# Kernel tuning notes

Hardware: AMD Instinct MI355X
Metric: run time of the kernel (lower is better)

The kernel has to match this reference:

```python
import jax, jax.numpy as jnp
import numpy as np

N = 100000   # nodes
E = 1600000  # edges (self-loop free by construction)
B = 512      # graphs in batch
F = 128      # input node features
HID = 128    # hidden dim
HEADS = 4
CH = HID // HEADS  # 32
EPS_BN = 1e-5


def setup_inputs() -> dict:
    key = jax.random.key(0)
    ks = jax.random.split(key, 24)
    x = jax.random.normal(ks[0], (N, F), jnp.float32)
    dst = jax.random.randint(ks[1], (E,), 0, N)
    off = jax.random.randint(ks[2], (E,), 1, N)
    src = (dst + off) % N  # guaranteed no self loops
    edge_index = jnp.stack([src, dst]).astype(jnp.int32)
    batch = jnp.sort(jax.random.randint(ks[3], (N,), 0, B)).astype(jnp.int32)
    g = lambda k, shape, fan: jax.random.normal(k, shape, jnp.float32) / np.sqrt(fan)
    return {
        "x": x, "edge_index": edge_index, "batch": batch,
        "W_in": g(ks[4], (F, HID), F), "b_in": jnp.zeros((HID,), jnp.float32),
        "lin_w": g(ks[5], (2, HID, HID), HID),
        "att_src": g(ks[6], (2, HEADS, CH), CH),
        "att_dst": g(ks[7], (2, HEADS, CH), CH),
        "conv_b": jnp.zeros((2, HID), jnp.float32),
        "lin_w_last": g(ks[8], (HID, HID), HID),
        "att_src_last": g(ks[9], (HID,), HID),
        "att_dst_last": g(ks[10], (HID,), HID),
        "b_last": jnp.zeros((HID,), jnp.float32),
        "bn_g": jnp.ones((3, HID), jnp.float32) + 0.1 * jax.random.normal(ks[11], (3, HID), jnp.float32),
        "bn_b": 0.1 * jax.random.normal(ks[12], (3, HID), jnp.float32),
        "bn_m": 0.1 * jax.random.normal(ks[13], (3, HID), jnp.float32),
        "bn_v": 0.5 + jax.random.uniform(ks[14], (3, HID), jnp.float32),
        "ro_w1": g(ks[15], (HID, HID // 2), HID),
        "ro_b1": jnp.zeros((HID // 2,), jnp.float32),
        "ro_w2": g(ks[16], (HID // 2, 1), HID // 2),
        "ro_b2": jnp.zeros((1,), jnp.float32),
    }


def _gat_conv(h, src, dst, W, a_src, a_dst, bias, concat):
    """PyG GATConv (shared lin for src/dst, add_self_loops=True, eval mode)."""
    n = h.shape[0]
    heads, ch = a_src.shape
    xs = (h @ W).reshape(n, heads, ch)              # [N,H,C]
    al_s = jnp.sum(xs * a_src, axis=-1)             # [N,H]
    al_d = jnp.sum(xs * a_dst, axis=-1)             # [N,H]
    loop = jnp.arange(n, dtype=src.dtype)
    src_f = jnp.concatenate([src, loop])
    dst_f = jnp.concatenate([dst, loop])
    e = jax.nn.leaky_relu(al_s[src_f] + al_d[dst_f], 0.2)   # [E+N,H]
    m = jax.ops.segment_max(e, dst_f, num_segments=n)       # dest-grouped softmax
    ee = jnp.exp(e - m[dst_f])
    z = jax.ops.segment_sum(ee, dst_f, num_segments=n)
    alpha = ee / (z[dst_f] + 1e-16)                          # [E+N,H]
    out = jax.ops.segment_sum(alpha[:, :, None] * xs[src_f], dst_f, num_segments=n)
    out = out.reshape(n, heads * ch) if concat else jnp.mean(out, axis=1)
    return out + bias


def _bn_eval(h, g, b, m, v):
    return (h - m) * (g / jnp.sqrt(v + EPS_BN)) + b


def _seg_softmax(scores, seg, num_segments):
    m = jax.ops.segment_max(scores, seg, num_segments=num_segments)
    e = jnp.exp(scores - m[seg])
    z = jax.ops.segment_sum(e, seg, num_segments=num_segments)
    return e / z[seg]


def reference(x, edge_index, batch, W_in, b_in, lin_w, att_src, att_dst, conv_b,
              lin_w_last, att_src_last, att_dst_last, b_last,
              bn_g, bn_b, bn_m, bn_v, ro_w1, ro_b1, ro_w2, ro_b2):
    src, dst = edge_index[0], edge_index[1]
    h = x @ W_in + b_in                                       # input_proj
    # first num_layers-1 multi-head concat layers
    for i in range(2):
        h_new = _gat_conv(h, src, dst, lin_w[i], att_src[i], att_dst[i], conv_b[i], True)
        h_new = jax.nn.elu(_bn_eval(h_new, bn_g[i], bn_b[i], bn_m[i], bn_v[i]))
        h = h + h_new                                         # residual (shapes match)
    # final single-head layer, concat=False
    h_new = _gat_conv(h, src, dst, lin_w_last, att_src_last[None, :], att_dst_last[None, :], b_last, False)
    h_new = jax.nn.elu(_bn_eval(h_new, bn_g[2], bn_b[2], bn_m[2], bn_v[2]))
    h = h + h_new
    # attention readout + per-graph softmax over atoms
    atom_scores = (jnp.tanh(h @ ro_w1 + ro_b1) @ ro_w2 + ro_b2)[:, 0]   # [N]
    atom_attention = _seg_softmax(atom_scores, batch, B)
    # attention-weighted add pool
    graph_emb = jax.ops.segment_sum(h * atom_attention[:, None], batch, num_segments=B)
    return graph_emb, atom_attention
```

## Files before the change

kernel.cpp:

```cpp
#include <hip/hip_runtime.h>
#include <math.h>
#include <stdint.h>

#define BSZ 512
#define BSH 9
#define NBKT_MAX 256

typedef __attribute__((ext_vector_type(8))) short bf16x8;
typedef __attribute__((ext_vector_type(4))) float f32x4;

static __device__ __forceinline__ uint32_t f2bf(float x) {
    uint32_t u = __float_as_uint(x);
    return (u + 0x7fffu + ((u >> 16) & 1u)) >> 16;
}
static __device__ __forceinline__ float bflo(uint32_t v) { return __uint_as_float(v << 16); }
static __device__ __forceinline__ float bfhi(uint32_t v) { return __uint_as_float(v & 0xffff0000u); }
static __device__ __forceinline__ void split2(float x, short& hi, short& lo) {
    uint32_t hb = f2bf(x);
    float hf = __uint_as_float(hb << 16);
    uint32_t lb = f2bf(x - hf);
    hi = (short)hb; lo = (short)lb;
}

__global__ __launch_bounds__(256) void k_bucket(const int* __restrict__ src, const int* __restrict__ dst,
                                                int* __restrict__ bcur, uint32_t* __restrict__ bucketed,
                                                int e, int cap) {
    __shared__ int hist[NBKT_MAX];
    __shared__ int cur[NBKT_MAX];
    int t = threadIdx.x;
    hist[t] = 0;
    __syncthreads();
    int base = blockIdx.x * 8192;
#pragma unroll 4
    for (int i = 0; i < 32; ++i) {
        int ei = base + i * 256 + t;
        if (ei < e) atomicAdd(&hist[dst[ei] >> BSH], 1);
    }
    __syncthreads();
    int hc = hist[t];
    cur[t] = (hc > 0) ? atomicAdd(&bcur[t], hc) : 0;
    __syncthreads();
#pragma unroll 4
    for (int i = 0; i < 32; ++i) {
        int ei = base + i * 256 + t;
        if (ei < e) {
            int d = dst[ei], s = src[ei];
            int b = d >> BSH;
            int p = atomicAdd(&cur[b], 1);
            if (p < (b + 1) * cap)
                bucketed[p] = ((uint32_t)(d & (BSZ - 1)) << 23) | (uint32_t)s;
        }
    }
}
__global__ __launch_bounds__(256) void k_bcount(const int* __restrict__ bcur, const uint32_t* __restrict__ bucketed,
                                                int* __restrict__ cnt, int n, int cap) {
    __shared__ int lf[BSZ];
    int b = blockIdx.x, t = threadIdx.x;
    int n0 = b << BSH;
    int nn = min(BSZ, n - n0);
    for (int i = t; i < nn; i += 256) lf[i] = 0;
    __syncthreads();
    int cb = min(bcur[b] - b * cap, cap);
    const uint32_t* ba = bucketed + (size_t)b * cap;
    for (int i = t; i < cb; i += 256) atomicAdd(&lf[ba[i] >> 23], 1);
    __syncthreads();
    for (int i = t; i < nn; i += 256) cnt[n0 + i] = lf[i] + 1;
}
__global__ __launch_bounds__(256) void k_scan1(const int* __restrict__ cnt, int* __restrict__ bsum, int n) {
    __shared__ int sd[256];
    int base = blockIdx.x * 1024, t = threadIdx.x;
    int s = 0;
#pragma unroll
    for (int i = 0; i < 4; ++i) {
        int idx = base + t * 4 + i;
        if (idx < n) s += (cnt[idx] + 3) & ~3;
    }
    sd[t] = s; __syncthreads();
    for (int o = 128; o; o >>= 1) {
        if (t < o) sd[t] += sd[t + o];
        __syncthreads();
    }
    if (t == 0) bsum[blockIdx.x] = sd[0];
}
__global__ void k_scan2(int* __restrict__ bsum, int nb) {
    __shared__ int sd[128];
    int t = threadIdx.x;
    int v = (t < nb) ? bsum[t] : 0;
    sd[t] = v; __syncthreads();
    for (int o = 1; o < 128; o <<= 1) {
        int u = (t >= o) ? sd[t - o] : 0;
        __syncthreads();
        sd[t] += u;
        __syncthreads();
    }
    if (t < nb) bsum[t] = sd[t] - v;
}
__global__ __launch_bounds__(256) void k_scan3(const int* __restrict__ cnt, const int* __restrict__ bsum,
                                               int* __restrict__ rp, int n) {
    __shared__ int sd[256];
    int base = blockIdx.x * 1024, t = threadIdx.x;
    int v[4]; int s = 0;
#pragma unroll
    for (int i = 0; i < 4; ++i) {
        int idx = base + t * 4 + i;
        v[i] = (idx < n) ? ((cnt[idx] + 3) & ~3) : 0;
        s += v[i];
    }
    sd[t] = s; __syncthreads();
    for (int o = 1; o < 256; o <<= 1) {
        int u = (t >= o) ? sd[t - o] : 0;
        __syncthreads();
        sd[t] += u;
        __syncthreads();
    }
    int excl = sd[t] - s + bsum[blockIdx.x];
#pragma unroll
    for (int i = 0; i < 4; ++i) {
        int idx = base + t * 4 + i;
        if (idx < n) rp[idx] = excl;
        excl += v[i];
        if (idx == n - 1) rp[n] = excl;
    }
}
__global__ __launch_bounds__(256) void k_bscatter(const int* __restrict__ bcur, const uint32_t* __restrict__ bucketed,
                                                  const int* __restrict__ rp, int* __restrict__ col,
                                                  int n, int cap) {
    __shared__ int lf[BSZ];
    __shared__ int rpl[BSZ];
    int b = blockIdx.x, t = threadIdx.x;
    int n0 = b << BSH;
    int nn = min(BSZ, n - n0);
    for (int i = t; i < nn; i += 256) {
        int r = rp[n0 + i];
        rpl[i] = r;
        lf[i] = 1;
        col[r] = n0 + i;
    }
    __syncthreads();
    int cb = min(bcur[b] - b * cap, cap);
    const uint32_t* ba = bucketed + (size_t)b * cap;
    for (int i = t; i < cb; i += 256) {
        uint32_t v = ba[i];
        int ld = (int)(v >> 23), s = (int)(v & 0x7fffffu);
        int o = atomicAdd(&lf[ld], 1);
        col[rpl[ld] + o] = s;
    }
    __syncthreads();
    for (int i = t; i < nn; i += 256) {
        int c = lf[i], end = (c + 3) & ~3;
        int r = rpl[i];
        for (int j = c; j < end; ++j) col[r + j] = -1;
    }
}
__global__ __launch_bounds__(256) void k_prep(const float* __restrict__ W_in, const float* __restrict__ lin_w,
                                              const float* __restrict__ lin_w_last,
                                              uint16_t* __restrict__ wfh, uint16_t* __restrict__ wfl,
                                              int* __restrict__ bcur, int nbkt, int cap,
                                              const float* __restrict__ conv_b, const float* __restrict__ b_last,
                                              const float* __restrict__ bn_g, const float* __restrict__ bn_b,
                                              const float* __restrict__ bn_m, const float* __restrict__ bn_v,
                                              float* __restrict__ sc, float* __restrict__ sh) {
    int b = blockIdx.x, t = threadIdx.x;
    if (b < 256) {
        int i = b * 256 + t;
        int m = i >> 14, e = i & 16383;
        const float* src = (m == 0) ? W_in : (m == 1) ? lin_w : (m == 2) ? (lin_w + 16384) : lin_w_last;
        float v = src[e];
        int k = e >> 7, n = e & 127;
        int kc = k >> 5, g = (k >> 3) & 3, j = k & 7, ct = n >> 4, cln = n & 15;
        int idx = m * 16384 + (((kc * 8 + ct) * 64) + g * 16 + cln) * 8 + j;
        short hi, lo;
        split2(v, hi, lo);
        wfh[idx] = hi; wfl[idx] = lo;
    } else if (b == 256) {
        if (t < nbkt) bcur[t] = t * cap;
    } else {
        for (int i = t; i < 384; i += 256) {
            int layer = i >> 7, c = i & 127;
            float bias = (layer < 2) ? conv_b[layer * 128 + c] : b_last[c];
            float s = bn_g[i] * __frsqrt_rn(bn_v[i] + 1e-5f);
            sc[i] = s;
            sh[i] = (bias - bn_m[i]) * s + bn_b[i];
        }
    }
}

template <int ATT, int OBF>
__global__ __launch_bounds__(256, 4) void k_gemm(
    const float* __restrict__ A, const uint16_t* __restrict__ wfh, const uint16_t* __restrict__ wfl,
    const float* __restrict__ bias, void* __restrict__ outv,
    const float* __restrict__ atts, const float* __restrict__ attd,
    float* __restrict__ als, float* __restrict__ ald, int nrows)
{
    __shared__ __align__(16) char smem[36864];
    const int t = threadIdx.x;
    const int l = t & 63, wv = t >> 6;
    const int cl = l & 15, gl = l >> 4;
    const int row0w = blockIdx.x * 64 + wv * 16;

    {
        const uint4* gh = (const uint4*)wfh;
        uint4* sh = (uint4*)smem;
#pragma unroll
        for (int i = 0; i < 8; ++i) sh[t + i * 256] = gh[t + i * 256];
    }

    float bloc[8], avsl[8], avdl[8];
    if (ATT == 0) {
#pragma unroll
        for (int ct = 0; ct < 8; ++ct) bloc[ct] = bias[ct * 16 + cl];
    } else {
#pragma unroll
        for (int ct = 0; ct < 8; ++ct) { avsl[ct] = atts[ct * 16 + cl]; avdl[ct] = attd[ct * 16 + cl]; }
    }

    bf16x8 Ah[4], Al[4];
    {
        int row = row0w + cl;
        bool ok = row < nrows;
        const float* ap = A + (size_t)row * 128 + gl * 8;
#pragma unroll
        for (int kc = 0; kc < 4; ++kc) {
            float4 u = make_float4(0.f, 0.f, 0.f, 0.f), v = u;
            if (ok) {
                u = *(const float4*)(ap + kc * 32);
                v = *(const float4*)(ap + kc * 32 + 4);
            }
            float xv[8] = {u.x, u.y, u.z, u.w, v.x, v.y, v.z, v.w};
            bf16x8 hbv, lbv;
#pragma unroll
            for (int j = 0; j < 8; ++j) {
                short hi, lo;
                split2(xv[j], hi, lo);
                hbv[j] = hi; lbv[j] = lo;
            }
            Ah[kc] = hbv; Al[kc] = lbv;
        }
    }
    __syncthreads();

    const uint16_t* WH = (const uint16_t*)smem;
    f32x4 acc[8];
#pragma unroll
    for (int ct = 0; ct < 8; ++ct) { f32x4 z = {0.f, 0.f, 0.f, 0.f}; acc[ct] = z; }
#pragma unroll
    for (int kc = 0; kc < 4; ++kc) {
#pragma unroll
        for (int ct = 0; ct < 8; ++ct) {
            bf16x8 bh = *(const bf16x8*)&WH[(((kc * 8 + ct) * 64) + l) * 8];
            bf16x8 bl = *(const bf16x8*)(wfl + (size_t)(((kc * 8 + ct) * 64) + l) * 8);
            acc[ct] = __builtin_amdgcn_mfma_f32_16x16x32_bf16(Ah[kc], bh, acc[ct], 0, 0, 0);
            acc[ct] = __builtin_amdgcn_mfma_f32_16x16x32_bf16(Ah[kc], bl, acc[ct], 0, 0, 0);
            acc[ct] = __builtin_amdgcn_mfma_f32_16x16x32_bf16(Al[kc], bh, acc[ct], 0, 0, 0);
        }
    }
    __syncthreads();

    if (OBF) {
        uint16_t* out = (uint16_t*)outv;
        uint16_t* buf = (uint16_t*)(smem + wv * 9216);
#pragma unroll
        for (int ct = 0; ct < 8; ++ct)
#pragma unroll
            for (int r = 0; r < 4; ++r)
                buf[(gl * 4 + r) * 152 + ct * 16 + cl] = (uint16_t)f2bf(acc[ct][r]);
#pragma unroll
        for (int ri = 0; ri < 4; ++ri) {
            int rloc = ri * 4 + gl;
            int row = row0w + rloc;
            if (row < nrows) {
                uint4 v = *(const uint4*)&buf[rloc * 152 + cl * 8];
                *(uint4*)&out[(size_t)row * 128 + cl * 8] = v;
            }
        }
    } else {
        float* out = (float*)outv;
        float* buf = (float*)(smem + wv * 9216);
#pragma unroll
        for (int ct = 0; ct < 8; ++ct)
#pragma unroll
            for (int r = 0; r < 4; ++r)
                buf[(gl * 4 + r) * 136 + ct * 16 + cl] = acc[ct][r] + bloc[ct];
#pragma unroll
        for (int ri = 0; ri < 4; ++ri) {
            int rloc = ri * 4 + gl;
            int row = row0w + rloc;
            if (row < nrows) {
                float4 v0 = *(const float4*)&buf[rloc * 136 + cl * 8];
                float4 v1 = *(const float4*)&buf[rloc * 136 + cl * 8 + 4];
                *(float4*)&out[(size_t)row * 128 + cl * 8] = v0;
                *(float4*)&out[(size_t)row * 128 + cl * 8 + 4] = v1;
            }
        }
    }

    if (ATT == 4) {
#pragma unroll
        for (int r = 0; r < 4; ++r) {
            float s[4], d[4];
#pragma unroll
            for (int hh = 0; hh < 4; ++hh) {
                s[hh] = acc[2 * hh][r] * avsl[2 * hh] + acc[2 * hh + 1][r] * avsl[2 * hh + 1];
                d[hh] = acc[2 * hh][r] * avdl[2 * hh] + acc[2 * hh + 1][r] * avdl[2 * hh + 1];
            }
#pragma unroll
            for (int hh = 0; hh < 4; ++hh) {
                s[hh] += __shfl_xor(s[hh], 1); s[hh] += __shfl_xor(s[hh], 2);
                s[hh] += __shfl_xor(s[hh], 4); s[hh] += __shfl_xor(s[hh], 8);
                d[hh] += __shfl_xor(d[hh], 1); d[hh] += __shfl_xor(d[hh], 2);
                d[hh] += __shfl_xor(d[hh], 4); d[hh] += __shfl_xor(d[hh], 8);
            }
            int row = row0w + gl * 4 + r;
            if (row < nrows && cl < 4) { als[row * 4 + cl] = s[cl]; ald[row * 4 + cl] = d[cl]; }
        }
    } else if (ATT == 1) {
#pragma unroll
        for (int r = 0; r < 4; ++r) {
            float s = 0.f, d = 0.f;
#pragma unroll
            for (int ct = 0; ct < 8; ++ct) {
                s += acc[ct][r] * avsl[ct];
                d += acc[ct][r] * avdl[ct];
            }
            s += __shfl_xor(s, 1); s += __shfl_xor(s, 2); s += __shfl_xor(s, 4); s += __shfl_xor(s, 8);
            d += __shfl_xor(d, 1); d += __shfl_xor(d, 2); d += __shfl_xor(d, 4); d += __shfl_xor(d, 8);
            int row = row0w + gl * 4 + r;
            if (row < nrows && cl == 0) { als[row] = s; ald[row] = d; }
        }
    }
}

template <int H>
__global__ __launch_bounds__(256) void k_agg(
    const int* __restrict__ rp, const int* __restrict__ col,
    const float* __restrict__ als, const float* __restrict__ ald_,
    const uint16_t* __restrict__ xs, const float* __restrict__ bnsc,
    const float* __restrict__ bnsh, float* __restrict__ h, int n)
{
    constexpr int EPG = (H == 4) ? 16 : 64;
    int node = blockIdx.x * 4 + (threadIdx.x >> 6);
    if (node >= n) return;
    int l = threadIdx.x & 63;
    int hl = (H == 4) ? (l >> 4) : 0;
    int lbase = (H == 4) ? (l & 48) : 0;
    int c0 = l * 2;
    float ad = ald_[node * H + hl];
    int jb = rp[node], je = rp[node + 1];
    float2 hv = *(const float2*)&h[(size_t)node * 128 + c0];
    float sc0v = bnsc[c0], sc1v = bnsc[c0 + 1];
    float sh0v = bnsh[c0], sh1v = bnsh[c0 + 1];

    float z = 0.f, a0 = 0.f, a1 = 0.f;
    for (int j = jb; j < je; j += EPG) {
        int e_l = j + (l & (EPG - 1));
        int s_l = (e_l < je) ? col[e_l] : -1;
        int t_l = s_l < 0 ? 0 : s_l;
        float lg = ((H == 4) ? als[t_l * 4 + hl] : als[t_l]) + ad;
        lg = fmaxf(lg, 0.2f * lg);
        float p_l = (s_l < 0) ? 0.f : __expf(lg);
        int ng = min(EPG, je - j);
        int q = 0;
        for (; q + 8 <= ng; q += 8) {
            int4 ca = *(const int4*)&col[j + q];
            int4 cb = *(const int4*)&col[j + q + 4];
            float p0 = __shfl(p_l, lbase | (q + 0));
            float p1 = __shfl(p_l, lbase | (q + 1));
            float p2 = __shfl(p_l, lbase | (q + 2));
            float p3 = __shfl(p_l, lbase | (q + 3));
            float p4 = __shfl(p_l, lbase | (q + 4));
            float p5 = __shfl(p_l, lbase | (q + 5));
            float p6 = __shfl(p_l, lbase | (q + 6));
            float p7 = __shfl(p_l, lbase | (q + 7));
            int t0 = max(ca.x, 0), t1 = max(ca.y, 0), t2 = max(ca.z, 0), t3 = max(ca.w, 0);
            int t4 = max(cb.x, 0), t5 = max(cb.y, 0), t6 = max(cb.z, 0), t7 = max(cb.w, 0);
            uint32_t x0 = *(const uint32_t*)(xs + (size_t)t0 * 128 + c0);
            uint32_t x1 = *(const uint32_t*)(xs + (size_t)t1 * 128 + c0);
            uint32_t x2 = *(const uint32_t*)(xs + (size_t)t2 * 128 + c0);
            uint32_t x3 = *(const uint32_t*)(xs + (size_t)t3 * 128 + c0);
            uint32_t x4 = *(const uint32_t*)(xs + (size_t)t4 * 128 + c0);
            uint32_t x5 = *(const uint32_t*)(xs + (size_t)t5 * 128 + c0);
            uint32_t x6 = *(const uint32_t*)(xs + (size_t)t6 * 128 + c0);
            uint32_t x7 = *(const uint32_t*)(xs + (size_t)t7 * 128 + c0);
            z += ((p0 + p1) + (p2 + p3)) + ((p4 + p5) + (p6 + p7));
            float s0 = fmaf(p0, bflo(x0), fmaf(p1, bflo(x1), fmaf(p2, bflo(x2), p3 * bflo(x3))));
            float s1 = fmaf(p4, bflo(x4), fmaf(p5, bflo(x5), fmaf(p6, bflo(x6), p7 * bflo(x7))));
            a0 += s0 + s1;
            float u0 = fmaf(p0, bfhi(x0), fmaf(p1, bfhi(x1), fmaf(p2, bfhi(x2), p3 * bfhi(x3))));
            float u1 = fmaf(p4, bfhi(x4), fmaf(p5, bfhi(x5), fmaf(p6, bfhi(x6), p7 * bfhi(x7))));
            a1 += u0 + u1;
        }
        if (q < ng) {
            int4 ca = *(const int4*)&col[j + q];
            float p0 = __shfl(p_l, lbase | (q + 0));
            float p1 = __shfl(p_l, lbase | (q + 1));
            float p2 = __shfl(p_l, lbase | (q + 2));
            float p3 = __shfl(p_l, lbase | (q + 3));
            int t0 = max(ca.x, 0), t1 = max(ca.y, 0), t2 = max(ca.z, 0), t3 = max(ca.w, 0);
            uint32_t x0 = *(const uint32_t*)(xs + (size_t)t0 * 128 + c0);
            uint32_t x1 = *(const uint32_t*)(xs + (size_t)t1 * 128 + c0);
            uint32_t x2 = *(const uint32_t*)(xs + (size_t)t2 * 128 + c0);
            uint32_t x3 = *(const uint32_t*)(xs + (size_t)t3 * 128 + c0);
            z += (p0 + p1) + (p2 + p3);
            a0 = fmaf(p0, bflo(x0), fmaf(p1, bflo(x1), fmaf(p2, bflo(x2), fmaf(p3, bflo(x3), a0))));
            a1 = fmaf(p0, bfhi(x0), fmaf(p1, bfhi(x1), fmaf(p2, bfhi(x2), fmaf(p3, bfhi(x3), a1))));
        }
    }
    float inv = 1.f / z;
    float y0 = fmaf(a0 * inv, sc0v, sh0v);
    float y1 = fmaf(a1 * inv, sc1v, sh1v);
    y0 = y0 > 0.f ? y0 : expm1f(y0);
    y1 = y1 > 0.f ? y1 : expm1f(y1);
    hv.x += y0; hv.y += y1;
    *(float2*)&h[(size_t)node * 128 + c0] = hv;
}

__global__ void k_graph_ptr(const int* __restrict__ batch, int* __restrict__ gptr, int n, int B) {
    int i = blockIdx.x * 256 + threadIdx.x;
    if (i >= n) return;
    int b = batch[i];
    int bp = (i == 0) ? -1 : batch[i - 1];
    for (int g = bp + 1; g <= b; ++g) gptr[g] = i;
    if (i == n - 1)
        for (int g = b + 1; g <= B; ++g) gptr[g] = n;
}

__global__ __launch_bounds__(256) void k_scores_pool(
    const int* __restrict__ gptr, const float* __restrict__ h,
    const float* __restrict__ w1, const float* __restrict__ b1,
    const float* __restrict__ w2, const float* __restrict__ b2,
    float* __restrict__ att, float* __restrict__ emb)
{
    __shared__ float W1s[128 * 64];
    __shared__ float As[16][132];
    __shared__ float red[4][32][4];
    __shared__ float sc[512];
    __shared__ float zred[4];
    const int t = threadIdx.x;
    const int g = blockIdx.x;
    const int s0g = gptr[g];
    const int s1g = gptr[g + 1];
    const int nn = min(s1g - s0g, 512);
    {
        const float4* w4 = (const float4*)w1;
        float4* s4 = (float4*)W1s;
#pragma unroll
        for (int i = 0; i < 8; ++i) s4[t + i * 256] = w4[t + i * 256];
    }
    const int rg = t & 31, cg = t >> 5;
    const int r0 = rg * 4, c0 = cg * 8;
    const int ar = (t * 2) >> 2;
    const int ak0 = ((t * 2) & 3) * 4, ak1 = ((t * 2 + 1) & 3) * 4;
    float bloc[8], w2loc[8];
#pragma unroll
    for (int j = 0; j < 8; ++j) { bloc[j] = b1[c0 + j]; w2loc[j] = w2[c0 + j]; }
    const float b2v = b2[0];

    for (int tile = 0; tile * 128 < nn; ++tile) {
        const int row0 = s0g + tile * 128;
        float acc[4][8] = {};
        for (int kc = 0; kc < 8; ++kc) {
            __syncthreads();
            {
                float4 v0 = make_float4(0.f, 0.f, 0.f, 0.f), v1 = v0;
                int row = row0 + ar;
                if (row < s1g) {
                    v0 = *(const float4*)&h[(size_t)row * 128 + kc * 16 + ak0];
                    v1 = *(const float4*)&h[(size_t)row * 128 + kc * 16 + ak1];
                }
                As[ak0 + 0][ar] = v0.x; As[ak0 + 1][ar] = v0.y; As[ak0 + 2][ar] = v0.z; As[ak0 + 3][ar] = v0.w;
                As[ak1 + 0][ar] = v1.x; As[ak1 + 1][ar] = v1.y; As[ak1 + 2][ar] = v1.z; As[ak1 + 3][ar] = v1.w;
            }
            __syncthreads();
#pragma unroll
            for (int kk = 0; kk < 16; ++kk) {
                float a[4], w[8];
                *(float4*)&a[0] = *(const float4*)&As[kk][r0];
                *(float4*)&w[0] = *(const float4*)&W1s[(kc * 16 + kk) * 64 + c0];
                *(float4*)&w[4] = *(const float4*)&W1s[(kc * 16 + kk) * 64 + c0 + 4];
#pragma unroll
                for (int r = 0; r < 4; ++r)
#pragma unroll
                    for (int j = 0; j < 8; ++j) acc[r][j] += a[r] * w[j];
            }
        }
        float part[4];
#pragma unroll
        for (int r = 0; r < 4; ++r) {
            float s = 0.f;
#pragma unroll
            for (int j = 0; j < 8; ++j) s += tanhf(acc[r][j] + bloc[j]) * w2loc[j];
            part[r] = s;
        }
#pragma unroll
        for (int r = 0; r < 4; ++r) part[r] += __shfl_xor(part[r], 32);
        const int wvi = t >> 6;
        if ((t & 32) == 0) {
#pragma unroll
            for (int r = 0; r < 4; ++r) red[wvi][rg][r] = part[r];
        }
        __syncthreads();
        if (t < 128) {
            int rl = tile * 128 + t;
            if (rl < nn) {
                float s = red[0][t >> 2][t & 3] + red[1][t >> 2][t & 3]
                        + red[2][t >> 2][t & 3] + red[3][t >> 2][t & 3];
                sc[rl] = s + b2v;
            }
        }
    }
    __syncthreads();
    float zl = 0.f;
    for (int i = t; i < nn; i += 256) zl += __expf(sc[i]);
#pragma unroll
    for (int off = 32; off; off >>= 1) zl += __shfl_xor(zl, off);
    if ((t & 63) == 0) zred[t >> 6] = zl;
    __syncthreads();
    float inv = 1.f / (zred[0] + zred[1] + zred[2] + zred[3]);
    float* sd = (float*)As;
    int p = t >> 4, cq = (t & 15) * 8;
    float4 acc0 = make_float4(0.f, 0.f, 0.f, 0.f), acc1 = acc0;
    for (int i = p; i < nn; i += 16) {
        float a = __expf(sc[i]) * inv;
        if ((t & 15) == 0) att[s0g + i] = a;
        float4 h0 = *(const float4*)&h[(size_t)(s0g + i) * 128 + cq];
        float4 h1 = *(const float4*)&h[(size_t)(s0g + i) * 128 + cq + 4];
        acc0.x += a * h0.x; acc0.y += a * h0.y; acc0.z += a * h0.z; acc0.w += a * h0.w;
        acc1.x += a * h1.x; acc1.y += a * h1.y; acc1.z += a * h1.z; acc1.w += a * h1.w;
    }
    *(float4*)&sd[p * 128 + cq] = acc0;
    *(float4*)&sd[p * 128 + cq + 4] = acc1;
    __syncthreads();
    if (t < 128) {
        float s = 0.f;
#pragma unroll
        for (int q = 0; q < 16; ++q) s += sd[q * 128 + t];
        emb[g * 128 + t] = s;
    }
}

extern "C" void kernel_launch(void* const* d_in, const int* in_sizes, int n_in,
                              void* d_out, int out_size, void* d_ws, size_t ws_size,
                              hipStream_t stream)
{
    const float* x            = (const float*)d_in[0];
    const int*   eidx         = (const int*)d_in[1];
    const int*   batch        = (const int*)d_in[2];
    const float* W_in         = (const float*)d_in[3];
    const float* b_in         = (const float*)d_in[4];
    const float* lin_w        = (const float*)d_in[5];
    const float* att_src      = (const float*)d_in[6];
    const float* att_dst      = (const float*)d_in[7];
    const float* conv_b       = (const float*)d_in[8];
    const float* lin_w_last   = (const float*)d_in[9];
    const float* att_src_last = (const float*)d_in[10];
    const float* att_dst_last = (const float*)d_in[11];
    const float* b_last       = (const float*)d_in[12];
    const float* bn_g         = (const float*)d_in[13];
    const float* bn_b         = (const float*)d_in[14];
    const float* bn_m         = (const float*)d_in[15];
    const float* bn_v         = (const float*)d_in[16];
    const float* ro_w1        = (const float*)d_in[17];
    const float* ro_b1        = (const float*)d_in[18];
    const float* ro_w2        = (const float*)d_in[19];
    const float* ro_b2        = (const float*)d_in[20];

    const int N = in_sizes[0] / 128;
    const int E = in_sizes[1] / 2;
    const int B = 512;
    const int* esrc = eidx;
    const int* edst = eidx + E;
    const int colcap = E + 4 * N + 64;
    const int NBKT = (N + BSZ - 1) >> BSH;
    const int cap = (E / NBKT) * 3 / 2 + 512;

    char* wsp = (char*)d_ws;
    size_t off = 0;
    auto alloc = [&](size_t bytes) -> void* {
        void* p = wsp + off;
        off += (bytes + 511) & ~(size_t)511;
        return p;
    };
    float*    h      = (float*)alloc((size_t)N * 128 * 4);
    uint16_t* xs     = (uint16_t*)alloc((size_t)N * 128 * 2);
    float*    als    = (float*)alloc((size_t)N * 4 * 4);
    float*    ald    = (float*)alloc((size_t)N * 4 * 4);
    int*      rp     = (int*)alloc((size_t)(N + 1) * 4);
    int*      col    = (int*)alloc((size_t)colcap * 4);
    int*      cnt    = (int*)alloc((size_t)N * 4);
    int*      bsum   = (int*)alloc(4096);
    int*      gptr   = (int*)alloc((size_t)(B + 1) * 4);
    float*    bnsc   = (float*)alloc(384 * 4);
    float*    bnsh   = (float*)alloc(384 * 4);
    int*      bcur   = (int*)alloc(NBKT_MAX * 4);
    uint16_t* wfh    = (uint16_t*)alloc(4 * 16384 * 2);
    uint16_t* wfl    = (uint16_t*)alloc(4 * 16384 * 2);
    uint32_t* bucketed = (uint32_t*)alloc((size_t)NBKT * cap * 4);
    (void)ws_size; (void)n_in; (void)out_size;

    float* emb = (float*)d_out;
    float* att = (float*)d_out + (size_t)B * 128;

    const int nb = (N + 1023) / 1024;
    hipLaunchKernelGGL(k_prep, dim3(258), dim3(256), 0, stream,
                       W_in, lin_w, lin_w_last, wfh, wfl, bcur, NBKT, cap,
                       conv_b, b_last, bn_g, bn_b, bn_m, bn_v, bnsc, bnsh);
    hipLaunchKernelGGL(k_bucket, dim3((E + 8191) / 8192), dim3(256), 0, stream,
                       esrc, edst, bcur, bucketed, E, cap);
    hipLaunchKernelGGL(k_bcount, dim3(NBKT), dim3(256), 0, stream, bcur, bucketed, cnt, N, cap);
    hipLaunchKernelGGL(k_scan1, dim3(nb), dim3(256), 0, stream, cnt, bsum, N);
    hipLaunchKernelGGL(k_scan2, dim3(1), dim3(128), 0, stream, bsum, nb);
    hipLaunchKernelGGL(k_scan3, dim3(nb), dim3(256), 0, stream, cnt, bsum, rp, N);
    hipLaunchKernelGGL(k_bscatter, dim3(NBKT), dim3(256), 0, stream, bcur, bucketed, rp, col, N, cap);

    const int ntiles = (N + 63) / 64;
    hipLaunchKernelGGL((k_gemm<0, 0>), dim3(ntiles), dim3(256), 0, stream,
                       x, wfh, wfl, b_in, (void*)h, (const float*)nullptr, (const float*)nullptr,
                       (float*)nullptr, (float*)nullptr, N);
    for (int i = 0; i < 2; ++i) {
        hipLaunchKernelGGL((k_gemm<4, 1>), dim3(ntiles), dim3(256), 0, stream,
                           h, wfh + (size_t)(i + 1) * 16384, wfl + (size_t)(i + 1) * 16384,
                           (const float*)nullptr, (void*)xs,
                           att_src + i * 128, att_dst + i * 128, als, ald, N);
        hipLaunchKernelGGL((k_agg<4>), dim3((N + 3) / 4), dim3(256), 0, stream,
                           rp, col, als, ald, xs, bnsc + i * 128, bnsh + i * 128, h, N);
    }
    hipLaunchKernelGGL((k_gemm<1, 1>), dim3(ntiles), dim3(256), 0, stream,
                       h, wfh + (size_t)3 * 16384, wfl + (size_t)3 * 16384,
                       (const float*)nullptr, (void*)xs,
                       att_src_last, att_dst_last, als, ald, N);
    hipLaunchKernelGGL((k_agg<1>), dim3((N + 3) / 4), dim3(256), 0, stream,
                       rp, col, als, ald, xs, bnsc + 256, bnsh + 256, h, N);

    hipLaunchKernelGGL(k_graph_ptr, dim3((N + 255) / 256), dim3(256), 0, stream, batch, gptr, N, B);
    hipLaunchKernelGGL(k_scores_pool, dim3(B), dim3(256), 0, stream,
                       gptr, h, ro_w1, ro_b1, ro_w2, ro_b2, att, emb);
}
```

Baseline: 470.6 us.

## Load GEMM weights into registers and process two row tiles per wave

The weight hi-part is no longer staged in LDS. Each wave now reads both hi and lo weight fragments straight from global memory (L2/L1) into registers once per k-chunk. Each wave covers 32 rows instead of 16, so every weight fragment feeds two row tiles, and the block covers 128 rows. This removes the LDS weight copy and its barriers and halves weight reads per row. The cost is much higher register pressure (two sets of accumulators and A fragments), which may lower occupancy now that the launch-bounds occupancy hint is dropped.

Result: slower. 487.0 us (+3.5%).

```diff
diff --git a/kernel.cpp b/kernel.cpp
--- a/kernel.cpp
+++ b/kernel.cpp
@@ -186,24 +186,17 @@
 }
 
 template <int ATT, int OBF>
-__global__ __launch_bounds__(256, 4) void k_gemm(
+__global__ __launch_bounds__(256) void k_gemm(
     const float* __restrict__ A, const uint16_t* __restrict__ wfh, const uint16_t* __restrict__ wfl,
     const float* __restrict__ bias, void* __restrict__ outv,
     const float* __restrict__ atts, const float* __restrict__ attd,
     float* __restrict__ als, float* __restrict__ ald, int nrows)
 {
-    __shared__ __align__(16) char smem[36864];
+    __shared__ __align__(16) char smem[4 * 16 * 152 * 2 > 4 * 16 * 136 * 4 ? 4 * 16 * 152 * 2 : 4 * 16 * 136 * 4];
     const int t = threadIdx.x;
     const int l = t & 63, wv = t >> 6;
     const int cl = l & 15, gl = l >> 4;
-    const int row0w = blockIdx.x * 64 + wv * 16;
-
-    {
-        const uint4* gh = (const uint4*)wfh;
-        uint4* sh = (uint4*)smem;
-#pragma unroll
-        for (int i = 0; i < 8; ++i) sh[t + i * 256] = gh[t + i * 256];
-    }
+    const int row0w = blockIdx.x * 128 + wv * 32;
 
     float bloc[8], avsl[8], avdl[8];
     if (ATT == 0) {
@@ -214,9 +207,10 @@
         for (int ct = 0; ct < 8; ++ct) { avsl[ct] = atts[ct * 16 + cl]; avdl[ct] = attd[ct * 16 + cl]; }
     }
 
-    bf16x8 Ah[4], Al[4];
-    {
-        int row = row0w + cl;
+    bf16x8 Ah[2][4], Al[2][4];
+#pragma unroll
+    for (int rt = 0; rt < 2; ++rt) {
+        int row = row0w + rt * 16 + cl;
         bool ok = row < nrows;
         const float* ap = A + (size_t)row * 128 + gl * 8;
 #pragma unroll
@@ -234,99 +228,114 @@
                 split2(xv[j], hi, lo);
                 hbv[j] = hi; lbv[j] = lo;
             }
-            Ah[kc] = hbv; Al[kc] = lbv;
-        }
-    }
-    __syncthreads();
-
-    const uint16_t* WH = (const uint16_t*)smem;
-    f32x4 acc[8];
-#pragma unroll
-    for (int ct = 0; ct < 8; ++ct) { f32x4 z = {0.f, 0.f, 0.f, 0.f}; acc[ct] = z; }
+            Ah[rt][kc] = hbv; Al[rt][kc] = lbv;
+        }
+    }
+
+    f32x4 acc[2][8];
+#pragma unroll
+    for (int rt = 0; rt < 2; ++rt)
+#pragma unroll
+        for (int ct = 0; ct < 8; ++ct) { f32x4 z = {0.f, 0.f, 0.f, 0.f}; acc[rt][ct] = z; }
 #pragma unroll
     for (int kc = 0; kc < 4; ++kc) {
+        bf16x8 bh[8], bl[8];
 #pragma unroll
         for (int ct = 0; ct < 8; ++ct) {
-            bf16x8 bh = *(const bf16x8*)&WH[(((kc * 8 + ct) * 64) + l) * 8];
-            bf16x8 bl = *(const bf16x8*)(wfl + (size_t)(((kc * 8 + ct) * 64) + l) * 8);
-            acc[ct] = __builtin_amdgcn_mfma_f32_16x16x32_bf16(Ah[kc], bh, acc[ct], 0, 0, 0);
-            acc[ct] = __builtin_amdgcn_mfma_f32_16x16x32_bf16(Ah[kc], bl, acc[ct], 0, 0, 0);
-            acc[ct] = __builtin_amdgcn_mfma_f32_16x16x32_bf16(Al[kc], bh, acc[ct], 0, 0, 0);
-        }
-    }
-    __syncthreads();
+            bh[ct] = *(const bf16x8*)(wfh + (size_t)(((kc * 8 + ct) * 64) + l) * 8);
+            bl[ct] = *(const bf16x8*)(wfl + (size_t)(((kc * 8 + ct) * 64) + l) * 8);
+        }
+#pragma unroll
+        for (int rt = 0; rt < 2; ++rt)
+#pragma unroll
+            for (int ct = 0; ct < 8; ++ct) {
+                acc[rt][ct] = __builtin_amdgcn_mfma_f32_16x16x32_bf16(Ah[rt][kc], bh[ct], acc[rt][ct], 0, 0, 0);
+                acc[rt][ct] = __builtin_amdgcn_mfma_f32_16x16x32_bf16(Ah[rt][kc], bl[ct], acc[rt][ct], 0, 0, 0);
+                acc[rt][ct] = __builtin_amdgcn_mfma_f32_16x16x32_bf16(Al[rt][kc], bh[ct], acc[rt][ct], 0, 0, 0);
+            }
+    }
 
     if (OBF) {
         uint16_t* out = (uint16_t*)outv;
-        uint16_t* buf = (uint16_t*)(smem + wv * 9216);
-#pragma unroll
-        for (int ct = 0; ct < 8; ++ct)
-#pragma unroll
-            for (int r = 0; r < 4; ++r)
-                buf[(gl * 4 + r) * 152 + ct * 16 + cl] = (uint16_t)f2bf(acc[ct][r]);
-#pragma unroll
-        for (int ri = 0; ri < 4; ++ri) {
-            int rloc = ri * 4 + gl;
-            int row = row0w + rloc;
-            if (row < nrows) {
-                uint4 v = *(const uint4*)&buf[rloc * 152 + cl * 8];
-                *(uint4*)&out[(size_t)row * 128 + cl * 8] = v;
+        uint16_t* buf = (uint16_t*)smem + wv * (16 * 152);
+#pragma unroll
+        for (int rt = 0; rt < 2; ++rt) {
+#pragma unroll
+            for (int ct = 0; ct < 8; ++ct)
+#pragma unroll
+                for (int r = 0; r < 4; ++r)
+                    buf[(gl * 4 + r) * 152 + ct * 16 + cl] = (uint16_t)f2bf(acc[rt][ct][r]);
+#pragma unroll
+            for (int ri = 0; ri < 4; ++ri) {
+                int rloc = ri * 4 + gl;
+                int row = row0w + rt * 16 + rloc;
+                if (row < nrows) {
+                    uint4 v = *(const uint4*)&buf[rloc * 152 + cl * 8];
+                    *(uint4*)&out[(size_t)row * 128 + cl * 8] = v;
+                }
             }
         }
     } else {
         float* out = (float*)outv;
-        float* buf = (float*)(smem + wv * 9216);
-#pragma unroll
-        for (int ct = 0; ct < 8; ++ct)
-#pragma unroll
-            for (int r = 0; r < 4; ++r)
-                buf[(gl * 4 + r) * 136 + ct * 16 + cl] = acc[ct][r] + bloc[ct];
-#pragma unroll
-        for (int ri = 0; ri < 4; ++ri) {
-            int rloc = ri * 4 + gl;
-            int row = row0w + rloc;
-            if (row < nrows) {
-                float4 v0 = *(const float4*)&buf[rloc * 136 + cl * 8];
-                float4 v1 = *(const float4*)&buf[rloc * 136 + cl * 8 + 4];
-                *(float4*)&out[(size_t)row * 128 + cl * 8] = v0;
-                *(float4*)&out[(size_t)row * 128 + cl * 8 + 4] = v1;
+        float* buf = (float*)smem + wv * (16 * 136);
+#pragma unroll
+        for (int rt = 0; rt < 2; ++rt) {
+#pragma unroll
+            for (int ct = 0; ct < 8; ++ct)
+#pragma unroll
+                for (int r = 0; r < 4; ++r)
+                    buf[(gl * 4 + r) * 136 + ct * 16 + cl] = acc[rt][ct][r] + bloc[ct];
+#pragma unroll
+            for (int ri = 0; ri < 4; ++ri) {
+                int rloc = ri * 4 + gl;
+                int row = row0w + rt * 16 + rloc;
+                if (row < nrows) {
+                    float4 v0 = *(const float4*)&buf[rloc * 136 + cl * 8];
+                    float4 v1 = *(const float4*)&buf[rloc * 136 + cl * 8 + 4];
+                    *(float4*)&out[(size_t)row * 128 + cl * 8] = v0;
+                    *(float4*)&out[(size_t)row * 128 + cl * 8 + 4] = v1;
+                }
             }
         }
     }
 
     if (ATT == 4) {
 #pragma unroll
-        for (int r = 0; r < 4; ++r) {
-            float s[4], d[4];
-#pragma unroll
-            for (int hh = 0; hh < 4; ++hh) {
-                s[hh] = acc[2 * hh][r] * avsl[2 * hh] + acc[2 * hh + 1][r] * avsl[2 * hh + 1];
-                d[hh] = acc[2 * hh][r] * avdl[2 * hh] + acc[2 * hh + 1][r] * avdl[2 * hh + 1];
-            }
-#pragma unroll
-            for (int hh = 0; hh < 4; ++hh) {
-                s[hh] += __shfl_xor(s[hh], 1); s[hh] += __shfl_xor(s[hh], 2);
-                s[hh] += __shfl_xor(s[hh], 4); s[hh] += __shfl_xor(s[hh], 8);
-                d[hh] += __shfl_xor(d[hh], 1); d[hh] += __shfl_xor(d[hh], 2);
-                d[hh] += __shfl_xor(d[hh], 4); d[hh] += __shfl_xor(d[hh], 8);
-            }
-            int row = row0w + gl * 4 + r;
-            if (row < nrows && cl < 4) { als[row * 4 + cl] = s[cl]; ald[row * 4 + cl] = d[cl]; }
-        }
+        for (int rt = 0; rt < 2; ++rt)
+#pragma unroll
+            for (int r = 0; r < 4; ++r) {
+                float s[4], d[4];
+#pragma unroll
+                for (int hh = 0; hh < 4; ++hh) {
+                    s[hh] = acc[rt][2 * hh][r] * avsl[2 * hh] + acc[rt][2 * hh + 1][r] * avsl[2 * hh + 1];
+                    d[hh] = acc[rt][2 * hh][r] * avdl[2 * hh] + acc[rt][2 * hh + 1][r] * avdl[2 * hh + 1];
+                }
+#pragma unroll
+                for (int hh = 0; hh < 4; ++hh) {
+                    s[hh] += __shfl_xor(s[hh], 1); s[hh] += __shfl_xor(s[hh], 2);
+                    s[hh] += __shfl_xor(s[hh], 4); s[hh] += __shfl_xor(s[hh], 8);
+                    d[hh] += __shfl_xor(d[hh], 1); d[hh] += __shfl_xor(d[hh], 2);
+                    d[hh] += __shfl_xor(d[hh], 4); d[hh] += __shfl_xor(d[hh], 8);
+                }
+                int row = row0w + rt * 16 + gl * 4 + r;
+                if (row < nrows && cl < 4) { als[row * 4 + cl] = s[cl]; ald[row * 4 + cl] = d[cl]; }
+            }
     } else if (ATT == 1) {
 #pragma unroll
-        for (int r = 0; r < 4; ++r) {
-            float s = 0.f, d = 0.f;
-#pragma unroll
-            for (int ct = 0; ct < 8; ++ct) {
-                s += acc[ct][r] * avsl[ct];
-                d += acc[ct][r] * avdl[ct];
-            }
-            s += __shfl_xor(s, 1); s += __shfl_xor(s, 2); s += __shfl_xor(s, 4); s += __shfl_xor(s, 8);
-            d += __shfl_xor(d, 1); d += __shfl_xor(d, 2); d += __shfl_xor(d, 4); d += __shfl_xor(d, 8);
-            int row = row0w + gl * 4 + r;
-            if (row < nrows && cl == 0) { als[row] = s; ald[row] = d; }
-        }
+        for (int rt = 0; rt < 2; ++rt)
+#pragma unroll
+            for (int r = 0; r < 4; ++r) {
+                float s = 0.f, d = 0.f;
+#pragma unroll
+                for (int ct = 0; ct < 8; ++ct) {
+                    s += acc[rt][ct][r] * avsl[ct];
+                    d += acc[rt][ct][r] * avdl[ct];
+                }
+                s += __shfl_xor(s, 1); s += __shfl_xor(s, 2); s += __shfl_xor(s, 4); s += __shfl_xor(s, 8);
+                d += __shfl_xor(d, 1); d += __shfl_xor(d, 2); d += __shfl_xor(d, 4); d += __shfl_xor(d, 8);
+                int row = row0w + rt * 16 + gl * 4 + r;
+                if (row < nrows && cl == 0) { als[row] = s; ald[row] = d; }
+            }
     }
 }
 
@@ -612,7 +621,7 @@
     hipLaunchKernelGGL(k_scan3, dim3(nb), dim3(256), 0, stream, cnt, bsum, rp, N);
     hipLaunchKernelGGL(k_bscatter, dim3(NBKT), dim3(256), 0, stream, bcur, bucketed, rp, col, N, cap);
 
-    const int ntiles = (N + 63) / 64;
+    const int ntiles = (N + 127) / 128;
     hipLaunchKernelGGL((k_gemm<0, 0>), dim3(ntiles), dim3(256), 0, stream,
                        x, wfh, wfl, b_in, (void*)h, (const float*)nullptr, (const float*)nullptr,
                        (float*)nullptr, (float*)nullptr, N);
```
